# Performance work log

Measured on AMD Instinct MI355X. Metric: run time of the kernel, lower is better.

## Reference

```python
import jax, jax.numpy as jnp
import numpy as np

PREF_DIM = 2
PREF_EMB = 64
HIDDEN = 512
NUM_CHUNKS = 105
CHUNK_EMB = 64
NUM_WS = 11
W_DIM = 20000


def setup_inputs() -> dict:
    key = jax.random.key(0)
    ks = jax.random.split(key, 12)
    in_dim = PREF_EMB + CHUNK_EMB
    inp = {
        "preference": jax.random.uniform(ks[0], (PREF_DIM,), dtype=jnp.float32),
        "pref_emb": 0.1 * jax.random.normal(ks[1], (PREF_DIM, PREF_EMB), dtype=jnp.float32),
        "chunk_emb": 0.1 * jax.random.normal(ks[2], (NUM_CHUNKS, CHUNK_EMB), dtype=jnp.float32),
        "W1": jax.random.normal(ks[3], (HIDDEN, in_dim), dtype=jnp.float32) / np.sqrt(in_dim),
        "b1": jnp.zeros((HIDDEN,), dtype=jnp.float32),
        "W2": jax.random.normal(ks[4], (HIDDEN, HIDDEN), dtype=jnp.float32) / np.sqrt(HIDDEN),
        "b2": jnp.zeros((HIDDEN,), dtype=jnp.float32),
        "W3": jax.random.normal(ks[5], (HIDDEN, HIDDEN), dtype=jnp.float32) / np.sqrt(HIDDEN),
        "b3": jnp.zeros((HIDDEN,), dtype=jnp.float32),
        "ws": 0.1 * jax.random.normal(ks[6], (NUM_WS, W_DIM, HIDDEN), dtype=jnp.float32),
    }
    return inp


def reference(preference, pref_emb, chunk_emb, W1, b1, W2, b2, W3, b3, ws):
    # pref_embedding = sum_i preference[i] * pref_emb[i]  -> [PREF_EMB]
    pref_embedding = preference @ pref_emb
    # Batch all chunks: concat(pref_embedding, chunk_emb[c]) -> [C, PREF_EMB+CHUNK_EMB]
    C = chunk_emb.shape[0]
    x = jnp.concatenate(
        [jnp.broadcast_to(pref_embedding, (C, pref_embedding.shape[0])), chunk_emb],
        axis=1,
    )
    # 3-layer MLP (Linear/ReLU/Linear/ReLU/Linear)
    h = jax.nn.relu(x @ W1.T + b1)
    h = jax.nn.relu(h @ W2.T + b2)
    rep = h @ W3.T + b3  # [C, HIDDEN]
    # Per chunk, concat over ws of F.linear(rep, w): [C, NUM_WS, W_DIM]
    out = jnp.einsum("ch,kwh->ckw", rep, ws)
    # Flat weight vector (original then reshapes contiguous slices into a dict;
    # that slicing is a pure view op on this vector)
    return out.reshape(-1)
```

## Files before the change

### kernel.cpp

```cpp
#include <hip/hip_runtime.h>


typedef __bf16 bf16x8 __attribute__((ext_vector_type(8)));
typedef float f32x4 __attribute__((ext_vector_type(4)));

#define NUM_CHUNKS 105
#define HIDDEN 512
#define N_COLS 220000
#define PAD_CHUNKS 112

__global__ void mlp_kernel(const float* __restrict__ pref,
                           const float* __restrict__ pref_emb,
                           const float* __restrict__ chunk_emb,
                           const float* __restrict__ W1, const float* __restrict__ b1,
                           const float* __restrict__ W2, const float* __restrict__ b2,
                           const float* __restrict__ W3, const float* __restrict__ b3,
                           __bf16* __restrict__ repf) {
  __shared__ float x[128];
  __shared__ float h1[512];
  __shared__ float h2[512];
  const int tid = threadIdx.x;
  const int c = blockIdx.x;
  const int t = c >> 4, mmc = c & 15;

  if (c >= NUM_CHUNKS) {
    for (int jj = tid; jj < 512; jj += 256) {
      const int ss = jj >> 5, qq = (jj >> 3) & 3, j = jj & 7;
      const long idx = (((long)(ss * 7 + t) * 4 + qq) * 16 + mmc) * 8 + j;
      repf[idx] = (__bf16)0.f;
    }
    return;
  }

  if (tid < 64) {
    x[tid] = pref[0] * pref_emb[tid] + pref[1] * pref_emb[64 + tid];
  } else if (tid < 128) {
    x[tid] = chunk_emb[c * 64 + (tid - 64)];
  }
  __syncthreads();

  for (int jj = tid; jj < 512; jj += 256) {
    float s = b1[jj];
    const f32x4* wr = (const f32x4*)(W1 + jj * 128);
#pragma unroll
    for (int i = 0; i < 32; ++i) {
      f32x4 w = wr[i];
      s += w[0] * x[i * 4 + 0] + w[1] * x[i * 4 + 1] +
           w[2] * x[i * 4 + 2] + w[3] * x[i * 4 + 3];
    }
    h1[jj] = fmaxf(s, 0.f);
  }
  __syncthreads();

  for (int jj = tid; jj < 512; jj += 256) {
    float s = b2[jj];
    const f32x4* wr = (const f32x4*)(W2 + jj * 512);
#pragma unroll 8
    for (int i = 0; i < 128; ++i) {
      f32x4 w = wr[i];
      s += w[0] * h1[i * 4 + 0] + w[1] * h1[i * 4 + 1] +
           w[2] * h1[i * 4 + 2] + w[3] * h1[i * 4 + 3];
    }
    h2[jj] = fmaxf(s, 0.f);
  }
  __syncthreads();

  for (int jj = tid; jj < 512; jj += 256) {
    float s = b3[jj];
    const f32x4* wr = (const f32x4*)(W3 + jj * 512);
#pragma unroll 8
    for (int i = 0; i < 128; ++i) {
      f32x4 w = wr[i];
      s += w[0] * h2[i * 4 + 0] + w[1] * h2[i * 4 + 1] +
           w[2] * h2[i * 4 + 2] + w[3] * h2[i * 4 + 3];
    }
    const int ss = jj >> 5, qq = (jj >> 3) & 3, j = jj & 7;
    const long idx = (((long)(ss * 7 + t) * 4 + qq) * 16 + mmc) * 8 + j;
    repf[idx] = (__bf16)s;
  }
}

__global__ __launch_bounds__(64) void gemm_ws(
    const float* __restrict__ ws,
    const bf16x8* __restrict__ repf,
    float* __restrict__ out) {
  const int lane = threadIdx.x;
  const int q = lane >> 4;
  const int mm = lane & 15;
  const long cb = (long)blockIdx.x * 32;
  const long col0 = cb + mm;
  const long col1 = col0 + 16;

  const f32x4* w0 = (const f32x4*)(ws + col0 * 512) + q * 2;
  const f32x4* w1 = (const f32x4*)(ws + col1 * 512) + q * 2;

  f32x4 acc0[7], acc1[7];
#pragma unroll
  for (int t = 0; t < 7; ++t) {
    acc0[t] = (f32x4){0.f, 0.f, 0.f, 0.f};
    acc1[t] = (f32x4){0.f, 0.f, 0.f, 0.f};
  }

  f32x4 X0[2], X1[2], Y0[2], Y1[2];
  bf16x8 A[7];

  X0[0] = __builtin_nontemporal_load(w0 + 0);
  X1[0] = __builtin_nontemporal_load(w0 + 1);
  Y0[0] = __builtin_nontemporal_load(w1 + 0);
  Y1[0] = __builtin_nontemporal_load(w1 + 1);
  {
    const bf16x8* ap = repf + lane;
#pragma unroll
    for (int t = 0; t < 7; ++t) A[t] = ap[t * 64];
  }
  X0[1] = __builtin_nontemporal_load(w0 + 8);
  X1[1] = __builtin_nontemporal_load(w0 + 9);
  Y0[1] = __builtin_nontemporal_load(w1 + 8);
  Y1[1] = __builtin_nontemporal_load(w1 + 9);

#pragma unroll
  for (int s = 0; s < 16; ++s) {
    const int slot = s & 1;
    f32x4 x0 = X0[slot], x1 = X1[slot], y0 = Y0[slot], y1 = Y1[slot];
    bf16x8 b0, b1;
#pragma unroll
    for (int j = 0; j < 4; ++j) {
      b0[j] = (__bf16)x0[j];
      b0[4 + j] = (__bf16)x1[j];
      b1[j] = (__bf16)y0[j];
      b1[4 + j] = (__bf16)y1[j];
    }
#pragma unroll
    for (int t = 0; t < 7; ++t) {
      acc0[t] = __builtin_amdgcn_mfma_f32_16x16x32_bf16(A[t], b0, acc0[t], 0, 0, 0);
      acc1[t] = __builtin_amdgcn_mfma_f32_16x16x32_bf16(A[t], b1, acc1[t], 0, 0, 0);
    }
    if (s < 15) {
      const bf16x8* ap = repf + (s + 1) * 448 + lane;
#pragma unroll
      for (int t = 0; t < 7; ++t) A[t] = ap[t * 64];
    }
    if (s < 14) {
      X0[slot] = __builtin_nontemporal_load(w0 + (s + 2) * 8);
      X1[slot] = __builtin_nontemporal_load(w0 + (s + 2) * 8 + 1);
      Y0[slot] = __builtin_nontemporal_load(w1 + (s + 2) * 8);
      Y1[slot] = __builtin_nontemporal_load(w1 + (s + 2) * 8 + 1);
    }
  }

#pragma unroll
  for (int t = 0; t < 7; ++t) {
    const int mbase = t * 16 + q * 4;
#pragma unroll
    for (int r = 0; r < 4; ++r) {
      const int m = mbase + r;
      if (m < NUM_CHUNKS) {
        __builtin_nontemporal_store(acc0[t][r], out + (long)m * N_COLS + col0);
        __builtin_nontemporal_store(acc1[t][r], out + (long)m * N_COLS + col1);
      }
    }
  }
}

extern "C" void kernel_launch(void* const* d_in, const int* in_sizes, int n_in,
                              void* d_out, int out_size, void* d_ws, size_t ws_size,
                              hipStream_t stream) {
  const float* pref      = (const float*)d_in[0];
  const float* pref_emb  = (const float*)d_in[1];
  const float* chunk_emb = (const float*)d_in[2];
  const float* W1 = (const float*)d_in[3];
  const float* b1 = (const float*)d_in[4];
  const float* W2 = (const float*)d_in[5];
  const float* b2 = (const float*)d_in[6];
  const float* W3 = (const float*)d_in[7];
  const float* b3 = (const float*)d_in[8];
  const float* ws = (const float*)d_in[9];
  float* out = (float*)d_out;
  __bf16* repf = (__bf16*)d_ws;

  mlp_kernel<<<PAD_CHUNKS, 256, 0, stream>>>(pref, pref_emb, chunk_emb,
                                             W1, b1, W2, b2, W3, b3, repf);
  gemm_ws<<<N_COLS / 32, 64, 0, stream>>>(ws, (const bf16x8*)d_ws, out);
}
```

Measured before the change: 735.4 us.

## Stage rep matrix in LDS per 4-wave block and deepen ws prefetch

The GEMM kernel now uses 256-thread blocks. Each block copies the whole bf16 rep matrix (112 KB) into shared memory with global_load_lds, so four waves share one copy instead of each wave reading it from global/L2. The ws prefetch pipeline goes from two stages to three, A fragments are double-buffered from LDS, and bounds checks cover the partial last block. The large LDS footprint limits occupancy to one block per CU, so latency hiding depends on the deeper prefetch, and each block pays an up-front 112 KB copy.

```diff
diff --git a/kernel.cpp b/kernel.cpp
--- a/kernel.cpp
+++ b/kernel.cpp
@@ -8,6 +8,7 @@
 #define HIDDEN 512
 #define N_COLS 220000
 #define PAD_CHUNKS 112
+#define REP_CHUNKS 7168
 
 __global__ void mlp_kernel(const float* __restrict__ pref,
                            const float* __restrict__ pref_emb,
@@ -80,19 +81,47 @@
   }
 }
 
-__global__ __launch_bounds__(64) void gemm_ws(
+__global__ __launch_bounds__(256, 1) void gemm_ws(
     const float* __restrict__ ws,
     const bf16x8* __restrict__ repf,
     float* __restrict__ out) {
-  const int lane = threadIdx.x;
+  __shared__ bf16x8 Alds[REP_CHUNKS];
+
+  const int tid = threadIdx.x;
+  const int lane = tid & 63;
+  const int wv = tid >> 6;
   const int q = lane >> 4;
   const int mm = lane & 15;
-  const long cb = (long)blockIdx.x * 32;
+
+#pragma unroll
+  for (int i = 0; i < 28; ++i) {
+    const bf16x8* g = repf + wv * 1792 + i * 64 + lane;
+    __builtin_amdgcn_global_load_lds(
+        (const __attribute__((address_space(1))) unsigned int*)g,
+        (__attribute__((address_space(3))) unsigned int*)&Alds[wv * 1792 + i * 64],
+        16, 0, 0);
+  }
+
+  const long cb = (long)blockIdx.x * 128 + wv * 32;
   const long col0 = cb + mm;
   const long col1 = col0 + 16;
-
-  const f32x4* w0 = (const f32x4*)(ws + col0 * 512) + q * 2;
-  const f32x4* w1 = (const f32x4*)(ws + col1 * 512) + q * 2;
+  const bool v0 = col0 < N_COLS;
+  const bool v1 = col1 < N_COLS;
+  const long cl0 = v0 ? col0 : 0;
+  const long cl1 = v1 ? col1 : 0;
+  const f32x4* w0 = (const f32x4*)(ws + cl0 * 512) + q * 2;
+  const f32x4* w1 = (const f32x4*)(ws + cl1 * 512) + q * 2;
+
+  f32x4 X0[3], X1[3], Y0[3], Y1[3];
+#pragma unroll
+  for (int p = 0; p < 3; ++p) {
+    X0[p] = __builtin_nontemporal_load(w0 + p * 8);
+    X1[p] = __builtin_nontemporal_load(w0 + p * 8 + 1);
+    Y0[p] = __builtin_nontemporal_load(w1 + p * 8);
+    Y1[p] = __builtin_nontemporal_load(w1 + p * 8 + 1);
+  }
+
+  __syncthreads();
 
   f32x4 acc0[7], acc1[7];
 #pragma unroll
@@ -101,26 +130,20 @@
     acc1[t] = (f32x4){0.f, 0.f, 0.f, 0.f};
   }
 
-  f32x4 X0[2], X1[2], Y0[2], Y1[2];
-  bf16x8 A[7];
-
-  X0[0] = __builtin_nontemporal_load(w0 + 0);
-  X1[0] = __builtin_nontemporal_load(w0 + 1);
-  Y0[0] = __builtin_nontemporal_load(w1 + 0);
-  Y1[0] = __builtin_nontemporal_load(w1 + 1);
-  {
-    const bf16x8* ap = repf + lane;
-#pragma unroll
-    for (int t = 0; t < 7; ++t) A[t] = ap[t * 64];
-  }
-  X0[1] = __builtin_nontemporal_load(w0 + 8);
-  X1[1] = __builtin_nontemporal_load(w0 + 9);
-  Y0[1] = __builtin_nontemporal_load(w1 + 8);
-  Y1[1] = __builtin_nontemporal_load(w1 + 9);
+  bf16x8 Aa[7], Ab[7];
+#pragma unroll
+  for (int t = 0; t < 7; ++t) Aa[t] = Alds[t * 64 + lane];
 
 #pragma unroll
   for (int s = 0; s < 16; ++s) {
-    const int slot = s & 1;
+    if (s < 15) {
+#pragma unroll
+      for (int t = 0; t < 7; ++t) {
+        if (s & 1) Aa[t] = Alds[(s + 1) * 448 + t * 64 + lane];
+        else       Ab[t] = Alds[(s + 1) * 448 + t * 64 + lane];
+      }
+    }
+    const int slot = s % 3;
     f32x4 x0 = X0[slot], x1 = X1[slot], y0 = Y0[slot], y1 = Y1[slot];
     bf16x8 b0, b1;
 #pragma unroll
@@ -132,19 +155,15 @@
     }
 #pragma unroll
     for (int t = 0; t < 7; ++t) {
-      acc0[t] = __builtin_amdgcn_mfma_f32_16x16x32_bf16(A[t], b0, acc0[t], 0, 0, 0);
-      acc1[t] = __builtin_amdgcn_mfma_f32_16x16x32_bf16(A[t], b1, acc1[t], 0, 0, 0);
-    }
-    if (s < 15) {
-      const bf16x8* ap = repf + (s + 1) * 448 + lane;
-#pragma unroll
-      for (int t = 0; t < 7; ++t) A[t] = ap[t * 64];
-    }
-    if (s < 14) {
-      X0[slot] = __builtin_nontemporal_load(w0 + (s + 2) * 8);
-      X1[slot] = __builtin_nontemporal_load(w0 + (s + 2) * 8 + 1);
-      Y0[slot] = __builtin_nontemporal_load(w1 + (s + 2) * 8);
-      Y1[slot] = __builtin_nontemporal_load(w1 + (s + 2) * 8 + 1);
+      bf16x8 a = (s & 1) ? Ab[t] : Aa[t];
+      acc0[t] = __builtin_amdgcn_mfma_f32_16x16x32_bf16(a, b0, acc0[t], 0, 0, 0);
+      acc1[t] = __builtin_amdgcn_mfma_f32_16x16x32_bf16(a, b1, acc1[t], 0, 0, 0);
+    }
+    if (s < 13) {
+      X0[slot] = __builtin_nontemporal_load(w0 + (s + 3) * 8);
+      X1[slot] = __builtin_nontemporal_load(w0 + (s + 3) * 8 + 1);
+      Y0[slot] = __builtin_nontemporal_load(w1 + (s + 3) * 8);
+      Y1[slot] = __builtin_nontemporal_load(w1 + (s + 3) * 8 + 1);
     }
   }
 
@@ -155,8 +174,8 @@
     for (int r = 0; r < 4; ++r) {
       const int m = mbase + r;
       if (m < NUM_CHUNKS) {
-        __builtin_nontemporal_store(acc0[t][r], out + (long)m * N_COLS + col0);
-        __builtin_nontemporal_store(acc1[t][r], out + (long)m * N_COLS + col1);
+        if (v0) __builtin_nontemporal_store(acc0[t][r], out + (long)m * N_COLS + col0);
+        if (v1) __builtin_nontemporal_store(acc1[t][r], out + (long)m * N_COLS + col1);
       }
     }
   }
@@ -180,5 +199,6 @@
 
   mlp_kernel<<<PAD_CHUNKS, 256, 0, stream>>>(pref, pref_emb, chunk_emb,
                                              W1, b1, W2, b2, W3, b3, repf);
-  gemm_ws<<<N_COLS / 32, 64, 0, stream>>>(ws, (const bf16x8*)d_ws, out);
+  const int nblk = (N_COLS + 127) / 128;
+  gemm_ws<<<nblk, 256, 0, stream>>>(ws, (const bf16x8*)d_ws, out);
 }
```

After: 719.6 us. -2.1%, faster.
